# Kernel optimization log

Measured on AMD Instinct MI355X. Metric: run time of the kernel, lower is better.

The kernel has to match this reference:

```python
import jax, jax.numpy as jnp
import numpy as np

N = 131072      # total nodes = num_graphs * numNodes
E = 2097152     # edges (avg degree 16)
C_IN = 64
HID = 64        # hiddenChannels
NODES = 128     # numNodes per graph
B = 1024        # num_graphs
NCLS = 4


def setup_inputs() -> dict:
    key = jax.random.key(0)
    ks = jax.random.split(key, 10)
    x = jax.random.normal(ks[0], (N, C_IN), jnp.float32)
    edge_index = jax.random.randint(ks[1], (2, E), 0, N, dtype=jnp.int32)
    edge_attr = jax.random.uniform(ks[2], (E,), jnp.float32)
    # GCNConv params (stored as [in, out]); PyG uses glorot init, bias zeros
    W1 = jax.random.normal(ks[3], (C_IN, 2 * HID), jnp.float32) * (1.0 / np.sqrt(C_IN))
    b1 = jnp.zeros((2 * HID,), jnp.float32)
    W2 = jax.random.normal(ks[4], (2 * HID, HID), jnp.float32) * (1.0 / np.sqrt(2 * HID))
    b2 = jnp.zeros((HID,), jnp.float32)
    Wfc = jax.random.normal(ks[5], (HID * NODES, NCLS), jnp.float32) * (1.0 / np.sqrt(HID * NODES))
    bfc = jnp.zeros((NCLS,), jnp.float32)
    return {"x": x, "edge_index": edge_index, "edge_attr": edge_attr,
            "W1": W1, "b1": b1, "W2": W2, "b2": b2, "Wfc": Wfc, "bfc": bfc}


def gcn_conv(x, src, dst, ew, W, b):
    # PyG GCNConv: add self-loops (weight 1), symmetric normalization,
    # linear transform, scatter-add aggregation at target nodes, + bias.
    loop = jnp.arange(N, dtype=src.dtype)
    s = jnp.concatenate([src, loop])
    d = jnp.concatenate([dst, loop])
    w = jnp.concatenate([ew, jnp.ones((N,), ew.dtype)])
    deg = jax.ops.segment_sum(w, d, num_segments=N)                  # [N]
    dis = jnp.where(deg > 0, jax.lax.rsqrt(jnp.maximum(deg, 1e-30)), 0.0)
    norm = dis[s] * w * dis[d]                                       # [E+N]
    h = x @ W                                                        # [N, out]
    msg = h[s] * norm[:, None]                                       # gather + scale
    out = jax.ops.segment_sum(msg, d, num_segments=N)                # scatter-add
    return out + b


def reference(x, edge_index, edge_attr, W1, b1, W2, b2, Wfc, bfc):
    src, dst = edge_index[0], edge_index[1]
    h = jax.nn.relu(gcn_conv(x, src, dst, edge_attr, W1, b1))
    h = jax.nn.relu(gcn_conv(h, src, dst, edge_attr, W2, b2))
    h = h.reshape(B, HID * NODES)
    logits = h @ Wfc + bfc
    return jax.nn.softmax(logits, axis=1)
```

## Files before the change

### kernel.cpp

```cpp
#include <hip/hip_runtime.h>

#define N_NODES 131072
#define NE      2097152
#define CIN     64
#define HID     64
#define H2X     128
#define NODESG  128
#define NGRAPH  1024
#define NCLS    4

#define NBUCK   256
#define NPB     512
#define HBLK    1024
#define EPB     2048
#define STAGE_CAP 10240
#define DEGSC   1048576.0f
#define DEGMASK ((1ull << 40) - 1)

typedef short bf16x8 __attribute__((ext_vector_type(8)));
typedef float f32x4  __attribute__((ext_vector_type(4)));

__device__ __forceinline__ unsigned short f2b(float f) {
    unsigned int u = __float_as_uint(f);
    return (unsigned short)((u + 0x7fffu + ((u >> 16) & 1u)) >> 16);
}
__device__ __forceinline__ unsigned int pack2(float a, float b) {
    return (unsigned int)f2b(a) | ((unsigned int)f2b(b) << 16);
}
__device__ __forceinline__ float blo(unsigned u) { return __uint_as_float(u << 16); }
__device__ __forceinline__ float bhi(unsigned u) { return __uint_as_float(u & 0xffff0000u); }


__global__ __launch_bounds__(256) void k_wswiz(
        const float* __restrict__ W1, const float* __restrict__ W2,
        unsigned short* __restrict__ wf1, unsigned short* __restrict__ wf2) {
    int tid = threadIdx.x;
    int b = blockIdx.x;
    int idx = (b & 3) * 256 + tid;
    if (b < 4) {
        int kt = idx >> 9, nt = (idx >> 6) & 7, l = idx & 63;
        int lm = l & 15, lq = l >> 4;
        unsigned pk[4];
        #pragma unroll
        for (int jp = 0; jp < 4; ++jp) {
            float w0 = W1[(kt*32 + lq*8 + 2*jp)     * H2X + nt*16 + lm];
            float w1 = W1[(kt*32 + lq*8 + 2*jp + 1) * H2X + nt*16 + lm];
            pk[jp] = pack2(w0, w1);
        }
        *(uint4*)&wf1[idx * 8] = make_uint4(pk[0], pk[1], pk[2], pk[3]);
    } else {
        int kt = idx >> 8, nt = (idx >> 6) & 3, l = idx & 63;
        int lm = l & 15, lq = l >> 4;
        unsigned pk[4];
        #pragma unroll
        for (int jp = 0; jp < 4; ++jp) {
            float w0 = W2[(kt*32 + lq*8 + 2*jp)     * HID + nt*16 + lm];
            float w1 = W2[(kt*32 + lq*8 + 2*jp + 1) * HID + nt*16 + lm];
            pk[jp] = pack2(w0, w1);
        }
        *(uint4*)&wf2[idx * 8] = make_uint4(pk[0], pk[1], pk[2], pk[3]);
    }
}


__global__ __launch_bounds__(256) void k_hist(const int* __restrict__ dst,
                                              int* __restrict__ hist) {
    __shared__ unsigned bh[NBUCK];
    int t = threadIdx.x;
    bh[t] = 0;
    __syncthreads();
    int base = blockIdx.x * EPB;
    #pragma unroll
    for (int k = 0; k < EPB / 256; ++k) {
        int d = dst[base + t + 256 * k];
        atomicAdd(&bh[d >> 9], 1u);
    }
    __syncthreads();
    hist[t * HBLK + blockIdx.x] = (int)bh[t];
}

__global__ void k_scan1(const int* __restrict__ in, int* __restrict__ out,
                        int* __restrict__ partial) {
    __shared__ int sd[256];
    int t = threadIdx.x;
    int base = blockIdx.x * 512;
    int c0 = in[base + 2*t];
    int c1 = in[base + 2*t + 1];
    int loc = c0 + c1;
    sd[t] = loc;
    __syncthreads();
    for (int off = 1; off < 256; off <<= 1) {
        int v = (t >= off) ? sd[t - off] : 0;
        __syncthreads();
        sd[t] += v;
        __syncthreads();
    }
    int excl = sd[t] - loc;
    out[base + 2*t]     = excl;
    out[base + 2*t + 1] = excl + c0;
    if (t == 255) partial[blockIdx.x] = sd[t];
}

__global__ void k_scan2(int* __restrict__ partial) {
    __shared__ int sd[256];
    int t = threadIdx.x;
    int p0 = partial[2*t], p1 = partial[2*t + 1];
    int loc = p0 + p1;
    sd[t] = loc;
    __syncthreads();
    for (int off = 1; off < 256; off <<= 1) {
        int v = (t >= off) ? sd[t - off] : 0;
        __syncthreads();
        sd[t] += v;
        __syncthreads();
    }
    int excl = sd[t] - loc;
    partial[2*t]     = excl;
    partial[2*t + 1] = excl + p0;
}

__global__ __launch_bounds__(256) void k_scatter(
        const int* __restrict__ src, const int* __restrict__ dst,
        const float* __restrict__ ew, const int* __restrict__ hist,
        const int* __restrict__ partial, unsigned long long* __restrict__ part) {
    __shared__ unsigned lcur[NBUCK];
    int t = threadIdx.x;
    int gi = t * HBLK + blockIdx.x;
    lcur[t] = (unsigned)(hist[gi] + partial[gi >> 9]);
    __syncthreads();
    int base = blockIdx.x * EPB;
    #pragma unroll
    for (int k = 0; k < EPB / 256; ++k) {
        int e = base + t + 256 * k;
        int s = src[e], d = dst[e];
        unsigned w = __float_as_uint(ew[e]);
        unsigned p = atomicAdd(&lcur[d >> 9], 1u);
        part[p] = ((unsigned long long)w << 32) |
                  ((unsigned long long)(unsigned)(d & 511) << 17) |
                  (unsigned long long)(unsigned)s;
    }
}

__global__ __launch_bounds__(256) void k_bucket(
        const unsigned long long* __restrict__ part, const int* __restrict__ hist,
        const int* __restrict__ partial, int2* __restrict__ csr,
        int* __restrict__ rowptr, int* __restrict__ counts, float* __restrict__ dis,
        const float* __restrict__ x, uint2* __restrict__ xb2) {
    __shared__ unsigned long long stage[STAGE_CAP];
    __shared__ unsigned long long dc[NPB];
    __shared__ unsigned cnt2[NPB];
    __shared__ int rp[NPB];
    __shared__ int sd[256];
    __shared__ float sdis[NPB];
    int t = threadIdx.x, b = blockIdx.x;
    dc[t] = 0; dc[t + 256] = 0;
    cnt2[t] = 0; cnt2[t + 256] = 0;
    __syncthreads();
    int start = hist[b * HBLK] + partial[2 * b];
    int end   = (b == NBUCK - 1) ? NE : (hist[(b + 1) * HBLK] + partial[2 * (b + 1)]);

    for (int j = start + t; j < end; j += 256) {
        unsigned long long p = part[j];
        int loc = j - start;
        if (loc < STAGE_CAP) stage[loc] = p;
        unsigned dl = (unsigned)(p >> 17) & 511u;
        float w = __uint_as_float((unsigned)(p >> 32));
        atomicAdd(&dc[dl], (1ull << 40) | (unsigned long long)(unsigned)(w * DEGSC));
    }
    __syncthreads();

    unsigned long long d0 = dc[2*t], d1 = dc[2*t + 1];
    int c0 = (int)(d0 >> 40), c1 = (int)(d1 >> 40);
    int loc = c0 + c1;
    sd[t] = loc;
    __syncthreads();
    for (int off = 1; off < 256; off <<= 1) {
        int v = (t >= off) ? sd[t - off] : 0;
        __syncthreads();
        sd[t] += v;
        __syncthreads();
    }
    int excl = sd[t] - loc;
    rp[2*t] = excl; rp[2*t + 1] = excl + c0;

    int n0 = b * NPB;
    rowptr[n0 + 2*t]     = start + excl;
    rowptr[n0 + 2*t + 1] = start + excl + c0;
    counts[n0 + 2*t]     = c0;
    counts[n0 + 2*t + 1] = c1;
    float dg0 = (float)(d0 & DEGMASK) * (1.0f / DEGSC);
    float dg1 = (float)(d1 & DEGMASK) * (1.0f / DEGSC);
    float di0 = rsqrtf(dg0 + 1.0f);
    float di1 = rsqrtf(dg1 + 1.0f);
    dis[n0 + 2*t]     = di0;
    dis[n0 + 2*t + 1] = di1;
    sdis[2*t]     = di0;
    sdis[2*t + 1] = di1;
    __syncthreads();

    for (int j = start + t; j < end; j += 256) {
        int lo = j - start;
        unsigned long long p = (lo < STAGE_CAP) ? stage[lo] : part[j];
        unsigned dl = (unsigned)(p >> 17) & 511u;
        int s = (int)(p & 0x1ffffu);
        unsigned r = atomicAdd(&cnt2[dl], 1u);
        csr[start + rp[dl] + (int)r] = make_int2(s, (int)(unsigned)(p >> 32));
    }

    const float4* x4 = (const float4*)x + (size_t)n0 * 16;
    uint2* y2 = xb2 + (size_t)n0 * 16;
    #pragma unroll 4
    for (int i = t; i < NPB * 16; i += 256) {
        float d = sdis[i >> 4];
        float4 v = x4[i];
        y2[i] = make_uint2(pack2(d * v.x, d * v.y), pack2(d * v.z, d * v.w));
    }
}


#define GATHER_PAIR(TAB, pA, pB, nA, nB, cmA, cmB, a0,a1,a2,a3, b0,b1,b2,b3, vSA, vSB) \
    {                                                                                  \
        int   sA0 = __shfl(pA.x, qid),      sA1 = __shfl(pA.x, qid + 4);               \
        int   sA2 = __shfl(pA.x, qid + 8),  sA3 = __shfl(pA.x, qid + 12);              \
        float fA0 = __int_as_float(__shfl(pA.y, qid));                                 \
        float fA1 = __int_as_float(__shfl(pA.y, qid + 4));                             \
        float fA2 = __int_as_float(__shfl(pA.y, qid + 8));                             \
        float fA3 = __int_as_float(__shfl(pA.y, qid + 12));                            \
        int   sB0 = __shfl(pB.x, qid),      sB1 = __shfl(pB.x, qid + 4);               \
        int   sB2 = __shfl(pB.x, qid + 8),  sB3 = __shfl(pB.x, qid + 12);              \
        float fB0 = __int_as_float(__shfl(pB.y, qid));                                 \
        float fB1 = __int_as_float(__shfl(pB.y, qid + 4));                             \
        float fB2 = __int_as_float(__shfl(pB.y, qid + 8));                             \
        float fB3 = __int_as_float(__shfl(pB.y, qid + 12));                            \
        uint2 vA0 = TAB[((unsigned)sA0 << 4) | ql];                                    \
        uint2 vA1 = TAB[((unsigned)sA1 << 4) | ql];                                    \
        uint2 vA2 = TAB[((unsigned)sA2 << 4) | ql];                                    \
        uint2 vA3 = TAB[((unsigned)sA3 << 4) | ql];                                    \
        uint2 vB0 = TAB[((unsigned)sB0 << 4) | ql];                                    \
        uint2 vB1 = TAB[((unsigned)sB1 << 4) | ql];                                    \
        uint2 vB2 = TAB[((unsigned)sB2 << 4) | ql];                                    \
        uint2 vB3 = TAB[((unsigned)sB3 << 4) | ql];                                    \
        vSA = TAB[((unsigned)nA << 4) | ql];                                           \
        vSB = TAB[((unsigned)nB << 4) | ql];                                           \
        a0 = fmaf(fA0, blo(vA0.x), a0); a1 = fmaf(fA0, bhi(vA0.x), a1);                \
        a2 = fmaf(fA0, blo(vA0.y), a2); a3 = fmaf(fA0, bhi(vA0.y), a3);                \
        a0 = fmaf(fA1, blo(vA1.x), a0); a1 = fmaf(fA1, bhi(vA1.x), a1);                \
        a2 = fmaf(fA1, blo(vA1.y), a2); a3 = fmaf(fA1, bhi(vA1.y), a3);                \
        a0 = fmaf(fA2, blo(vA2.x), a0); a1 = fmaf(fA2, bhi(vA2.x), a1);                \
        a2 = fmaf(fA2, blo(vA2.y), a2); a3 = fmaf(fA2, bhi(vA2.y), a3);                \
        a0 = fmaf(fA3, blo(vA3.x), a0); a1 = fmaf(fA3, bhi(vA3.x), a1);                \
        a2 = fmaf(fA3, blo(vA3.y), a2); a3 = fmaf(fA3, bhi(vA3.y), a3);                \
        b0 = fmaf(fB0, blo(vB0.x), b0); b1 = fmaf(fB0, bhi(vB0.x), b1);                \
        b2 = fmaf(fB0, blo(vB0.y), b2); b3 = fmaf(fB0, bhi(vB0.y), b3);                \
        b0 = fmaf(fB1, blo(vB1.x), b0); b1 = fmaf(fB1, bhi(vB1.x), b1);                \
        b2 = fmaf(fB1, blo(vB1.y), b2); b3 = fmaf(fB1, bhi(vB1.y), b3);                \
        b0 = fmaf(fB2, blo(vB2.x), b0); b1 = fmaf(fB2, bhi(vB2.x), b1);                \
        b2 = fmaf(fB2, blo(vB2.y), b2); b3 = fmaf(fB2, bhi(vB2.y), b3);                \
        b0 = fmaf(fB3, blo(vB3.x), b0); b1 = fmaf(fB3, bhi(vB3.x), b1);                \
        b2 = fmaf(fB3, blo(vB3.y), b2); b3 = fmaf(fB3, bhi(vB3.y), b3);                \
        int tsA = (cmA > 16) ? ((cmA - 13) >> 2) : 0;                                  \
        int tsB = (cmB > 16) ? ((cmB - 13) >> 2) : 0;                                  \
        int tsM = tsA > tsB ? tsA : tsB;                                               \
        if (tsM > 0) {                                                                 \
            int jj0 = 16 + qid;                                                        \
            float tfA = __int_as_float(__shfl(pA.y, jj0));                             \
            float tfB = __int_as_float(__shfl(pB.y, jj0));                             \
            uint2 tvA = TAB[((unsigned)__shfl(pA.x, jj0) << 4) | ql];                  \
            uint2 tvB = TAB[((unsigned)__shfl(pB.x, jj0) << 4) | ql];                  \
            for (int k = 1; k < tsM; ++k) {                                            \
                int jj = 16 + 4 * k + qid;                                             \
                float nfA = __int_as_float(__shfl(pA.y, jj));                          \
                float nfB = __int_as_float(__shfl(pB.y, jj));                          \
                uint2 nvA = TAB[((unsigned)__shfl(pA.x, jj) << 4) | ql];               \
                uint2 nvB = TAB[((unsigned)__shfl(pB.x, jj) << 4) | ql];               \
                a0 = fmaf(tfA, blo(tvA.x), a0); a1 = fmaf(tfA, bhi(tvA.x), a1);        \
                a2 = fmaf(tfA, blo(tvA.y), a2); a3 = fmaf(tfA, bhi(tvA.y), a3);        \
                b0 = fmaf(tfB, blo(tvB.x), b0); b1 = fmaf(tfB, bhi(tvB.x), b1);        \
                b2 = fmaf(tfB, blo(tvB.y), b2); b3 = fmaf(tfB, bhi(tvB.y), b3);        \
                tfA = nfA; tfB = nfB; tvA = nvA; tvB = nvB;                            \
            }                                                                          \
            a0 = fmaf(tfA, blo(tvA.x), a0); a1 = fmaf(tfA, bhi(tvA.x), a1);            \
            a2 = fmaf(tfA, blo(tvA.y), a2); a3 = fmaf(tfA, bhi(tvA.y), a3);            \
            b0 = fmaf(tfB, blo(tvB.x), b0); b1 = fmaf(tfB, bhi(tvB.x), b1);            \
            b2 = fmaf(tfB, blo(tvB.y), b2); b3 = fmaf(tfB, bhi(tvB.y), b3);            \
        }                                                                              \
        a0 += __shfl_xor(a0, 16); a1 += __shfl_xor(a1, 16);                            \
        a2 += __shfl_xor(a2, 16); a3 += __shfl_xor(a3, 16);                            \
        a0 += __shfl_xor(a0, 32); a1 += __shfl_xor(a1, 32);                            \
        a2 += __shfl_xor(a2, 32); a3 += __shfl_xor(a3, 32);                            \
        b0 += __shfl_xor(b0, 16); b1 += __shfl_xor(b1, 16);                            \
        b2 += __shfl_xor(b2, 16); b3 += __shfl_xor(b3, 16);                            \
        b0 += __shfl_xor(b0, 32); b1 += __shfl_xor(b1, 32);                            \
        b2 += __shfl_xor(b2, 32); b3 += __shfl_xor(b3, 32);                            \
    }


__global__ __launch_bounds__(256, 8) void k_layer1(
        const uint2* __restrict__ xb2, const int2* __restrict__ csr,
        const int* __restrict__ rowptr, const int* __restrict__ counts,
        const float* __restrict__ dis, const unsigned short* __restrict__ wf1,
        const unsigned short* __restrict__ wf2, const float* __restrict__ b1,
        unsigned short* __restrict__ t2u) {
    __shared__ unsigned short smem[32 * 136];
    unsigned short (*sagg_b)[72]  = (unsigned short (*)[72])smem;
    unsigned short (*sh1)[136]    = (unsigned short (*)[136])smem;
    int tid = threadIdx.x;

    int wave = tid >> 6, lane = tid & 63;
    int qid = lane >> 4, ql = lane & 15;
    int n0 = blockIdx.x * 32;
    int nb = n0 + wave * 8;

    #pragma unroll 1
    for (int ip = 0; ip < 8; ip += 2) {
        int nA = nb + ip, nB = nA + 1;
        int cA = counts[nA], cB = counts[nB];
        int rsA = rowptr[nA], rsB = rowptr[nB];
        float dnA = dis[nA], dnB = dis[nB];
        int cmA = cA < 64 ? cA : 64, cmB = cB < 64 ? cB : 64;
        int2 pA = (lane < cmA) ? csr[rsA + lane] : make_int2(0, 0);
        int2 pB = (lane < cmB) ? csr[rsB + lane] : make_int2(0, 0);
        float a0 = 0.f, a1 = 0.f, a2 = 0.f, a3 = 0.f;
        float b0 = 0.f, b1v = 0.f, b2v = 0.f, b3 = 0.f;
        uint2 vSA, vSB;
        GATHER_PAIR(xb2, pA, pB, nA, nB, cmA, cmB,
                    a0, a1, a2, a3, b0, b1v, b2v, b3, vSA, vSB);
        if (cA > 64) {
            for (int jj = 64; jj < cA; ++jj) {
                int2 p = csr[rsA + jj];
                float f = __int_as_float(p.y);
                uint2 v = xb2[((unsigned)p.x << 4) | ql];
                if (qid == 0) {
                    a0 += f * blo(v.x); a1 += f * bhi(v.x);
                    a2 += f * blo(v.y); a3 += f * bhi(v.y);
                }
            }
        }
        if (cB > 64) {
            for (int jj = 64; jj < cB; ++jj) {
                int2 p = csr[rsB + jj];
                float f = __int_as_float(p.y);
                uint2 v = xb2[((unsigned)p.x << 4) | ql];
                if (qid == 0) {
                    b0 += f * blo(v.x); b1v += f * bhi(v.x);
                    b2v += f * blo(v.y); b3 += f * bhi(v.y);
                }
            }
        }
        if (qid == 0) {
            int m = wave * 8 + ip;
            *(uint2*)&sagg_b[m][ql * 4] =
                make_uint2(pack2(dnA * (a0 + blo(vSA.x)), dnA * (a1 + bhi(vSA.x))),
                           pack2(dnA * (a2 + blo(vSA.y)), dnA * (a3 + bhi(vSA.y))));
            *(uint2*)&sagg_b[m + 1][ql * 4] =
                make_uint2(pack2(dnB * (b0 + blo(vSB.x)), dnB * (b1v + bhi(vSB.x))),
                           pack2(dnB * (b2v + blo(vSB.y)), dnB * (b3 + bhi(vSB.y))));
        }
    }
    __syncthreads();

    int mt = wave & 1, ntb = (wave >> 1) * 4;
    int lm = lane & 15, lq = lane >> 4;
    float bs[4];
    #pragma unroll
    for (int t = 0; t < 4; ++t) bs[t] = b1[(ntb + t) * 16 + lm];
    bf16x8 af0 = *(const bf16x8*)&sagg_b[mt*16 + lm][lq * 8];
    bf16x8 af1 = *(const bf16x8*)&sagg_b[mt*16 + lm][32 + lq * 8];
    __syncthreads();
    #pragma unroll
    for (int t = 0; t < 4; ++t) {
        int nt = ntb + t;
        bf16x8 bf0 = *(const bf16x8*)&wf1[(nt*64 + lane) * 8];
        bf16x8 bf1 = *(const bf16x8*)&wf1[((8 + nt)*64 + lane) * 8];
        f32x4 acc = {0.f, 0.f, 0.f, 0.f};
        acc = __builtin_amdgcn_mfma_f32_16x16x32_bf16(af0, bf0, acc, 0, 0, 0);
        acc = __builtin_amdgcn_mfma_f32_16x16x32_bf16(af1, bf1, acc, 0, 0, 0);
        int ch = nt*16 + lm;
        float bias = bs[t];
        #pragma unroll
        for (int r = 0; r < 4; ++r)
            sh1[mt*16 + lq*4 + r][ch] = f2b(fmaxf(acc[r] + bias, 0.f));
    }
    __syncthreads();

    #pragma unroll
    for (int ti = 0; ti < 2; ++ti) {
        int t = wave * 2 + ti;
        int mt2 = t & 1, nt2 = t >> 1;
        f32x4 acc = {0.f, 0.f, 0.f, 0.f};
        #pragma unroll
        for (int kt = 0; kt < 4; ++kt) {
            bf16x8 af = *(const bf16x8*)&sh1[mt2*16 + lm][kt*32 + lq*8];
            bf16x8 bf = *(const bf16x8*)&wf2[((kt*4 + nt2)*64 + lane) * 8];
            acc = __builtin_amdgcn_mfma_f32_16x16x32_bf16(af, bf, acc, 0, 0, 0);
        }
        int ch = nt2*16 + lm;
        #pragma unroll
        for (int r = 0; r < 4; ++r) {
            int node = n0 + mt2*16 + lq*4 + r;
            t2u[(size_t)node * HID + ch] = f2b(dis[node] * acc[r]);
        }
    }
}


__global__ __launch_bounds__(256, 8) void k_agg2(
        const uint2* __restrict__ t2y, const int2* __restrict__ csr,
        const int* __restrict__ rowptr, const int* __restrict__ counts,
        const float* __restrict__ dis, const float* __restrict__ b2,
        unsigned short* __restrict__ h2b) {
    int tid = threadIdx.x;
    int wave = tid >> 6, lane = tid & 63;
    int qid = lane >> 4, ql = lane & 15;
    float4 bb = *(const float4*)&b2[ql * 4];
    int n0 = blockIdx.x * 32;
    int nb = n0 + wave * 8;

    #pragma unroll 1
    for (int ip = 0; ip < 8; ip += 2) {
        int nA = nb + ip, nB = nA + 1;
        int cA = counts[nA], cB = counts[nB];
        int rsA = rowptr[nA], rsB = rowptr[nB];
        float dnA = dis[nA], dnB = dis[nB];
        int cmA = cA < 64 ? cA : 64, cmB = cB < 64 ? cB : 64;
        int2 pA = (lane < cmA) ? csr[rsA + lane] : make_int2(0, 0);
        int2 pB = (lane < cmB) ? csr[rsB + lane] : make_int2(0, 0);
        float a0 = 0.f, a1 = 0.f, a2 = 0.f, a3 = 0.f;
        float b0 = 0.f, b1v = 0.f, b2v = 0.f, b3 = 0.f;
        uint2 vSA, vSB;
        GATHER_PAIR(t2y, pA, pB, nA, nB, cmA, cmB,
                    a0, a1, a2, a3, b0, b1v, b2v, b3, vSA, vSB);
        if (cA > 64) {
            for (int jj = 64; jj < cA; ++jj) {
                int2 p = csr[rsA + jj];
                float f = __int_as_float(p.y);
                uint2 v = t2y[((unsigned)p.x << 4) | ql];
                if (qid == 0) {
                    a0 += f * blo(v.x); a1 += f * bhi(v.x);
                    a2 += f * blo(v.y); a3 += f * bhi(v.y);
                }
            }
        }
        if (cB > 64) {
            for (int jj = 64; jj < cB; ++jj) {
                int2 p = csr[rsB + jj];
                float f = __int_as_float(p.y);
                uint2 v = t2y[((unsigned)p.x << 4) | ql];
                if (qid == 0) {
                    b0 += f * blo(v.x); b1v += f * bhi(v.x);
                    b2v += f * blo(v.y); b3 += f * bhi(v.y);
                }
            }
        }
        if (qid == 0) {
            float oa0 = fmaxf(fmaf(dnA, a0 + blo(vSA.x), bb.x), 0.f);
            float oa1 = fmaxf(fmaf(dnA, a1 + bhi(vSA.x), bb.y), 0.f);
            float oa2 = fmaxf(fmaf(dnA, a2 + blo(vSA.y), bb.z), 0.f);
            float oa3 = fmaxf(fmaf(dnA, a3 + bhi(vSA.y), bb.w), 0.f);
            float ob0 = fmaxf(fmaf(dnB, b0 + blo(vSB.x), bb.x), 0.f);
            float ob1 = fmaxf(fmaf(dnB, b1v + bhi(vSB.x), bb.y), 0.f);
            float ob2 = fmaxf(fmaf(dnB, b2v + blo(vSB.y), bb.z), 0.f);
            float ob3 = fmaxf(fmaf(dnB, b3 + bhi(vSB.y), bb.w), 0.f);
            *(uint2*)&h2b[((unsigned)nA << 6) | (ql * 4)] =
                make_uint2(pack2(oa0, oa1), pack2(oa2, oa3));
            *(uint2*)&h2b[((unsigned)nB << 6) | (ql * 4)] =
                make_uint2(pack2(ob0, ob1), pack2(ob2, ob3));
        }
    }
}


__global__ __launch_bounds__(256) void k_fc(
        const unsigned short* __restrict__ h2b, const float* __restrict__ Wfc,
        const float* __restrict__ bfc, float* __restrict__ out) {
    __shared__ float4 red[256];
    int b = blockIdx.x, t = threadIdx.x;
    const uint2* hrow = (const uint2*)(h2b + (size_t)b * (HID * NODESG));
    const float4* W4 = (const float4*)Wfc;
    float4 a = make_float4(0.f, 0.f, 0.f, 0.f);
    #pragma unroll
    for (int j = 0; j < 8; ++j) {
        int i = j * 256 + t;
        uint2 hv = hrow[i];
        float h0 = blo(hv.x), h1 = bhi(hv.x), h2v = blo(hv.y), h3 = bhi(hv.y);
        float4 w0 = W4[i * 4 + 0];
        float4 w1 = W4[i * 4 + 1];
        float4 w2 = W4[i * 4 + 2];
        float4 w3 = W4[i * 4 + 3];
        a.x = fmaf(h0, w0.x, a.x); a.y = fmaf(h0, w0.y, a.y);
        a.z = fmaf(h0, w0.z, a.z); a.w = fmaf(h0, w0.w, a.w);
        a.x = fmaf(h1, w1.x, a.x); a.y = fmaf(h1, w1.y, a.y);
        a.z = fmaf(h1, w1.z, a.z); a.w = fmaf(h1, w1.w, a.w);
        a.x = fmaf(h2v, w2.x, a.x); a.y = fmaf(h2v, w2.y, a.y);
        a.z = fmaf(h2v, w2.z, a.z); a.w = fmaf(h2v, w2.w, a.w);
        a.x = fmaf(h3, w3.x, a.x); a.y = fmaf(h3, w3.y, a.y);
        a.z = fmaf(h3, w3.z, a.z); a.w = fmaf(h3, w3.w, a.w);
    }
    red[t] = a;
    __syncthreads();
    for (int s = 128; s > 0; s >>= 1) {
        if (t < s) {
            red[t].x += red[t + s].x; red[t].y += red[t + s].y;
            red[t].z += red[t + s].z; red[t].w += red[t + s].w;
        }
        __syncthreads();
    }
    if (t == 0) {
        float l0 = red[0].x + bfc[0];
        float l1 = red[0].y + bfc[1];
        float l2 = red[0].z + bfc[2];
        float l3 = red[0].w + bfc[3];
        float mx = fmaxf(fmaxf(l0, l1), fmaxf(l2, l3));
        float e0 = expf(l0 - mx), e1 = expf(l1 - mx);
        float e2 = expf(l2 - mx), e3 = expf(l3 - mx);
        float inv = 1.f / (e0 + e1 + e2 + e3);
        float4 o = make_float4(e0 * inv, e1 * inv, e2 * inv, e3 * inv);
        *(float4*)&out[(size_t)b * 4] = o;
    }
}


extern "C" void kernel_launch(void* const* d_in, const int* in_sizes, int n_in,
                              void* d_out, int out_size, void* d_ws, size_t ws_size,
                              hipStream_t stream) {
    const float* x   = (const float*)d_in[0];
    const int*   ei  = (const int*)  d_in[1];
    const float* ea  = (const float*)d_in[2];
    const float* W1  = (const float*)d_in[3];
    const float* b1  = (const float*)d_in[4];
    const float* W2  = (const float*)d_in[5];
    const float* b2  = (const float*)d_in[6];
    const float* Wfc = (const float*)d_in[7];
    const float* bfc = (const float*)d_in[8];
    float* out = (float*)d_out;
    const int* src = ei;
    const int* dst = ei + NE;

    char* ws = (char*)d_ws;
    size_t off = 0;
    int*   hist   = (int*)  (ws + off); off += (size_t)NBUCK * HBLK * 4;
    int*   partial= (int*)  (ws + off); off += 4096;
    int*   counts = (int*)  (ws + off); off += (size_t)N_NODES * 4;
    int*   rowptr = (int*)  (ws + off); off += (size_t)N_NODES * 4;
    float* dis    = (float*)(ws + off); off += (size_t)N_NODES * 4;
    unsigned short* wf1 = (unsigned short*)(ws + off); off += 8192 * 2;
    unsigned short* wf2 = (unsigned short*)(ws + off); off += 8192 * 2;
    int2*  csr    = (int2*) (ws + off); off += (size_t)NE * 8;
    uint2* xb2    = (uint2*)(ws + off); off += (size_t)N_NODES * CIN * 2;
    unsigned short* t2u = (unsigned short*)(ws + off); off += (size_t)N_NODES * HID * 2;
    unsigned short* h2b = (unsigned short*)(ws + off); off += (size_t)N_NODES * HID * 2;
    unsigned long long* part = (unsigned long long*)t2u;

    hipMemsetAsync(hist, 0, (size_t)NBUCK * HBLK * 4 + 4096, stream);

    k_wswiz  <<<8, 256, 0, stream>>>(W1, W2, wf1, wf2);
    k_hist   <<<HBLK, 256, 0, stream>>>(dst, hist);
    k_scan1  <<<NBUCK * HBLK / 512, 256, 0, stream>>>(hist, hist, partial);
    k_scan2  <<<1, 256, 0, stream>>>(partial);
    k_scatter<<<HBLK, 256, 0, stream>>>(src, dst, ea, hist, partial, part);
    k_bucket <<<NBUCK, 256, 0, stream>>>(part, hist, partial, csr, rowptr, counts,
                                         dis, x, xb2);
    k_layer1 <<<N_NODES / 32, 256, 0, stream>>>(xb2, csr, rowptr, counts, dis,
                                                wf1, wf2, b1, t2u);
    k_agg2   <<<N_NODES / 32, 256, 0, stream>>>((const uint2*)t2u, csr, rowptr,
                                                counts, dis, b2, h2b);
    k_fc     <<<NGRAPH, 256, 0, stream>>>(h2b, Wfc, bfc, out);
}
```

Measured before the change: 262.1 us.

## Merge weight swizzle into histogram kernel, fold partial scan into consumers, drop memset

Folds the weight-swizzle kernel into the histogram launch as extra blocks and removes the single-block partial-scan kernel: each scatter and bucket block now recomputes the 512-entry prefix scan of partials in shared memory. The hipMemsetAsync goes away because every hist entry is fully written. The FC reduction switches from a shared-memory tree to wave shuffles plus a 4-entry combine. The goal is fewer launches and fewer barriers, paid for with redundant per-block scan work in the scatter and bucket kernels.

```diff
diff --git a/kernel.cpp b/kernel.cpp
--- a/kernel.cpp
+++ b/kernel.cpp
@@ -31,52 +31,51 @@
 __device__ __forceinline__ float bhi(unsigned u) { return __uint_as_float(u & 0xffff0000u); }
 
 
-__global__ __launch_bounds__(256) void k_wswiz(
+__global__ __launch_bounds__(256) void k_hist(
+        const int* __restrict__ dst, int* __restrict__ hist,
         const float* __restrict__ W1, const float* __restrict__ W2,
         unsigned short* __restrict__ wf1, unsigned short* __restrict__ wf2) {
-    int tid = threadIdx.x;
+    int t = threadIdx.x;
     int b = blockIdx.x;
-    int idx = (b & 3) * 256 + tid;
-    if (b < 4) {
-        int kt = idx >> 9, nt = (idx >> 6) & 7, l = idx & 63;
-        int lm = l & 15, lq = l >> 4;
-        unsigned pk[4];
-        #pragma unroll
-        for (int jp = 0; jp < 4; ++jp) {
-            float w0 = W1[(kt*32 + lq*8 + 2*jp)     * H2X + nt*16 + lm];
-            float w1 = W1[(kt*32 + lq*8 + 2*jp + 1) * H2X + nt*16 + lm];
-            pk[jp] = pack2(w0, w1);
-        }
-        *(uint4*)&wf1[idx * 8] = make_uint4(pk[0], pk[1], pk[2], pk[3]);
-    } else {
-        int kt = idx >> 8, nt = (idx >> 6) & 3, l = idx & 63;
-        int lm = l & 15, lq = l >> 4;
-        unsigned pk[4];
-        #pragma unroll
-        for (int jp = 0; jp < 4; ++jp) {
-            float w0 = W2[(kt*32 + lq*8 + 2*jp)     * HID + nt*16 + lm];
-            float w1 = W2[(kt*32 + lq*8 + 2*jp + 1) * HID + nt*16 + lm];
-            pk[jp] = pack2(w0, w1);
-        }
-        *(uint4*)&wf2[idx * 8] = make_uint4(pk[0], pk[1], pk[2], pk[3]);
-    }
-}
-
-
-__global__ __launch_bounds__(256) void k_hist(const int* __restrict__ dst,
-                                              int* __restrict__ hist) {
+    if (b >= HBLK) {
+        int bb = b - HBLK;
+        int idx = (bb & 3) * 256 + t;
+        if (bb < 4) {
+            int kt = idx >> 9, nt = (idx >> 6) & 7, l = idx & 63;
+            int lm = l & 15, lq = l >> 4;
+            unsigned pk[4];
+            #pragma unroll
+            for (int jp = 0; jp < 4; ++jp) {
+                float w0 = W1[(kt*32 + lq*8 + 2*jp)     * H2X + nt*16 + lm];
+                float w1 = W1[(kt*32 + lq*8 + 2*jp + 1) * H2X + nt*16 + lm];
+                pk[jp] = pack2(w0, w1);
+            }
+            *(uint4*)&wf1[idx * 8] = make_uint4(pk[0], pk[1], pk[2], pk[3]);
+        } else {
+            int kt = idx >> 8, nt = (idx >> 6) & 3, l = idx & 63;
+            int lm = l & 15, lq = l >> 4;
+            unsigned pk[4];
+            #pragma unroll
+            for (int jp = 0; jp < 4; ++jp) {
+                float w0 = W2[(kt*32 + lq*8 + 2*jp)     * HID + nt*16 + lm];
+                float w1 = W2[(kt*32 + lq*8 + 2*jp + 1) * HID + nt*16 + lm];
+                pk[jp] = pack2(w0, w1);
+            }
+            *(uint4*)&wf2[idx * 8] = make_uint4(pk[0], pk[1], pk[2], pk[3]);
+        }
+        return;
+    }
     __shared__ unsigned bh[NBUCK];
-    int t = threadIdx.x;
     bh[t] = 0;
     __syncthreads();
-    int base = blockIdx.x * EPB;
+    int base = b * EPB;
     #pragma unroll
     for (int k = 0; k < EPB / 256; ++k) {
         int d = dst[base + t + 256 * k];
         atomicAdd(&bh[d >> 9], 1u);
     }
     __syncthreads();
-    hist[t * HBLK + blockIdx.x] = (int)bh[t];
+    hist[t * HBLK + b] = (int)bh[t];
 }
 
 __global__ void k_scan1(const int* __restrict__ in, int* __restrict__ out,
@@ -101,32 +100,34 @@
     if (t == 255) partial[blockIdx.x] = sd[t];
 }
 
-__global__ void k_scan2(int* __restrict__ partial) {
-    __shared__ int sd[256];
-    int t = threadIdx.x;
-    int p0 = partial[2*t], p1 = partial[2*t + 1];
-    int loc = p0 + p1;
-    sd[t] = loc;
-    __syncthreads();
-    for (int off = 1; off < 256; off <<= 1) {
-        int v = (t >= off) ? sd[t - off] : 0;
-        __syncthreads();
-        sd[t] += v;
-        __syncthreads();
-    }
-    int excl = sd[t] - loc;
-    partial[2*t]     = excl;
-    partial[2*t + 1] = excl + p0;
-}
+#define LOCAL_PSCAN(partial, sp, sd, t)                                        \
+    {                                                                          \
+        int p0 = partial[2*t], p1 = partial[2*t + 1];                          \
+        int loc = p0 + p1;                                                     \
+        sd[t] = loc;                                                           \
+        __syncthreads();                                                       \
+        for (int off = 1; off < 256; off <<= 1) {                              \
+            int v = (t >= off) ? sd[t - off] : 0;                              \
+            __syncthreads();                                                   \
+            sd[t] += v;                                                        \
+            __syncthreads();                                                   \
+        }                                                                      \
+        int excl = sd[t] - loc;                                                \
+        sp[2*t] = excl; sp[2*t + 1] = excl + p0;                               \
+        __syncthreads();                                                       \
+    }
 
 __global__ __launch_bounds__(256) void k_scatter(
         const int* __restrict__ src, const int* __restrict__ dst,
         const float* __restrict__ ew, const int* __restrict__ hist,
         const int* __restrict__ partial, unsigned long long* __restrict__ part) {
     __shared__ unsigned lcur[NBUCK];
+    __shared__ int sp[512];
+    __shared__ int sd[256];
     int t = threadIdx.x;
+    LOCAL_PSCAN(partial, sp, sd, t);
     int gi = t * HBLK + blockIdx.x;
-    lcur[t] = (unsigned)(hist[gi] + partial[gi >> 9]);
+    lcur[t] = (unsigned)(hist[gi] + sp[gi >> 9]);
     __syncthreads();
     int base = blockIdx.x * EPB;
     #pragma unroll
@@ -151,13 +152,15 @@
     __shared__ unsigned cnt2[NPB];
     __shared__ int rp[NPB];
     __shared__ int sd[256];
+    __shared__ int sp[512];
     __shared__ float sdis[NPB];
     int t = threadIdx.x, b = blockIdx.x;
     dc[t] = 0; dc[t + 256] = 0;
     cnt2[t] = 0; cnt2[t + 256] = 0;
-    __syncthreads();
-    int start = hist[b * HBLK] + partial[2 * b];
-    int end   = (b == NBUCK - 1) ? NE : (hist[(b + 1) * HBLK] + partial[2 * (b + 1)]);
+    LOCAL_PSCAN(partial, sp, sd, t);
+    int start = hist[b * HBLK] + sp[2 * b];
+    int end   = (b == NBUCK - 1) ? NE : (hist[(b + 1) * HBLK] + sp[2 * (b + 1)]);
+    __syncthreads();
 
     for (int j = start + t; j < end; j += 256) {
         unsigned long long p = part[j];
@@ -473,8 +476,9 @@
 __global__ __launch_bounds__(256) void k_fc(
         const unsigned short* __restrict__ h2b, const float* __restrict__ Wfc,
         const float* __restrict__ bfc, float* __restrict__ out) {
-    __shared__ float4 red[256];
+    __shared__ float4 red[4];
     int b = blockIdx.x, t = threadIdx.x;
+    int wave = t >> 6, lane = t & 63;
     const uint2* hrow = (const uint2*)(h2b + (size_t)b * (HID * NODESG));
     const float4* W4 = (const float4*)Wfc;
     float4 a = make_float4(0.f, 0.f, 0.f, 0.f);
@@ -496,20 +500,20 @@
         a.x = fmaf(h3, w3.x, a.x); a.y = fmaf(h3, w3.y, a.y);
         a.z = fmaf(h3, w3.z, a.z); a.w = fmaf(h3, w3.w, a.w);
     }
-    red[t] = a;
-    __syncthreads();
-    for (int s = 128; s > 0; s >>= 1) {
-        if (t < s) {
-            red[t].x += red[t + s].x; red[t].y += red[t + s].y;
-            red[t].z += red[t + s].z; red[t].w += red[t + s].w;
-        }
-        __syncthreads();
-    }
+    #pragma unroll
+    for (int off = 1; off < 64; off <<= 1) {
+        a.x += __shfl_xor(a.x, off);
+        a.y += __shfl_xor(a.y, off);
+        a.z += __shfl_xor(a.z, off);
+        a.w += __shfl_xor(a.w, off);
+    }
+    if (lane == 0) red[wave] = a;
+    __syncthreads();
     if (t == 0) {
-        float l0 = red[0].x + bfc[0];
-        float l1 = red[0].y + bfc[1];
-        float l2 = red[0].z + bfc[2];
-        float l3 = red[0].w + bfc[3];
+        float l0 = red[0].x + red[1].x + red[2].x + red[3].x + bfc[0];
+        float l1 = red[0].y + red[1].y + red[2].y + red[3].y + bfc[1];
+        float l2 = red[0].z + red[1].z + red[2].z + red[3].z + bfc[2];
+        float l3 = red[0].w + red[1].w + red[2].w + red[3].w + bfc[3];
         float mx = fmaxf(fmaxf(l0, l1), fmaxf(l2, l3));
         float e0 = expf(l0 - mx), e1 = expf(l1 - mx);
         float e2 = expf(l2 - mx), e3 = expf(l3 - mx);
@@ -551,12 +555,8 @@
     unsigned short* h2b = (unsigned short*)(ws + off); off += (size_t)N_NODES * HID * 2;
     unsigned long long* part = (unsigned long long*)t2u;
 
-    hipMemsetAsync(hist, 0, (size_t)NBUCK * HBLK * 4 + 4096, stream);
-
-    k_wswiz  <<<8, 256, 0, stream>>>(W1, W2, wf1, wf2);
-    k_hist   <<<HBLK, 256, 0, stream>>>(dst, hist);
+    k_hist   <<<HBLK + 8, 256, 0, stream>>>(dst, hist, W1, W2, wf1, wf2);
     k_scan1  <<<NBUCK * HBLK / 512, 256, 0, stream>>>(hist, hist, partial);
-    k_scan2  <<<1, 256, 0, stream>>>(partial);
     k_scatter<<<HBLK, 256, 0, stream>>>(src, dst, ea, hist, partial, part);
     k_bucket <<<NBUCK, 256, 0, stream>>>(part, hist, partial, csr, rowptr, counts,
                                          dis, x, xb2);
```

Measured after the change: 256.9 us. -2.0%, faster.
